# Optimization experiments

Hardware: AMD Instinct MI355X
Metric: run time of the kernel (lower is better)

The kernel has to match this reference:

```python
import jax, jax.numpy as jnp
import numpy as np

B = 16        # number of point clouds
NP = 4096     # points per cloud
RATIO = 0.25
RADIUS = 0.2
K = 64        # max_num_neighbors hardcoded in the torch module
S = int(NP * RATIO)  # sampled centers per cloud
C_IN = 64


def setup_inputs() -> dict:
    key = jax.random.key(0)
    ks = jax.random.split(key, 6)
    x = jax.random.normal(ks[0], (B * NP, C_IN), dtype=jnp.float32)
    pos = jax.random.uniform(ks[1], (B * NP, 3), dtype=jnp.float32)  # unit cube
    batch = jnp.repeat(jnp.arange(B, dtype=jnp.int64), NP)
    d0, d1, d2, d3 = C_IN + 3, 64, 64, 128  # local_nn dims
    W1 = jax.random.normal(ks[2], (d0, d1), dtype=jnp.float32) / np.sqrt(d0)
    W2 = jax.random.normal(ks[3], (d1, d2), dtype=jnp.float32) / np.sqrt(d1)
    W3 = jax.random.normal(ks[4], (d2, d3), dtype=jnp.float32) / np.sqrt(d2)
    b1 = jnp.zeros((d1,), jnp.float32)
    b2 = jnp.zeros((d2,), jnp.float32)
    b3 = jnp.zeros((d3,), jnp.float32)
    return {"x": x, "pos": pos, "batch": batch,
            "W1": W1, "b1": b1, "W2": W2, "b2": b2, "W3": W3, "b3": b3}


def _fps(pos_b):
    """Farthest point sampling for one cloud. pos_b: [NP,3] -> [S] int32 indices."""
    dmin = jnp.sum((pos_b - pos_b[0]) ** 2, axis=-1)  # start from point 0

    def step(dmin, _):
        idx = jnp.argmax(dmin).astype(jnp.int32)
        dmin = jnp.minimum(dmin, jnp.sum((pos_b - pos_b[idx]) ** 2, axis=-1))
        return dmin, idx

    _, idxs = jax.lax.scan(step, dmin, None, length=S - 1)
    return jnp.concatenate([jnp.zeros((1,), jnp.int32), idxs])


def reference(x, pos, batch, W1, b1, W2, b2, W3, b3):
    xb = x.reshape(B, NP, -1)
    pb = pos.reshape(B, NP, 3)

    def per_cloud(xb_, pb_):
        idxs = _fps(pb_)                      # [S]
        centers = pb_[idxs]                   # [S,3]
        # ball query: up to K nearest neighbors within RADIUS (center itself always in-range)
        d2 = jnp.sum((centers[:, None, :] - pb_[None, :, :]) ** 2, axis=-1)  # [S,NP]
        neg = jnp.where(d2 <= RADIUS * RADIUS, -d2, -jnp.inf)
        vals, nbr = jax.lax.top_k(neg, K)     # [S,K]
        valid = jnp.isfinite(vals)            # [S,K]
        # PointConv message: local_nn(concat(x_j, pos_j - pos_i)), max-aggregated
        xj = xb_[nbr]                         # [S,K,C]
        rel = pb_[nbr] - centers[:, None, :]  # [S,K,3]
        h = jnp.concatenate([xj, rel], axis=-1)
        h = jax.nn.relu(h @ W1 + b1)
        h = jax.nn.relu(h @ W2 + b2)
        h = h @ W3 + b3                       # [S,K,Cout]
        h = jnp.where(valid[..., None], h, -jnp.inf)
        return jnp.max(h, axis=1), centers    # [S,Cout], [S,3]

    out, centers = jax.vmap(per_cloud)(xb, pb)
    x_out = out.reshape(B * S, -1)
    pos_out = centers.reshape(B * S, 3)
    batch_out = jnp.repeat(jnp.arange(B, dtype=batch.dtype), S)
    return x_out, pos_out, batch_out
```

## Files before the change

### kernel.cpp

```cpp
#include <hip/hip_runtime.h>
#include <math.h>

#define NB   16
#define NPTS 4096
#define SS   1024
#define KK   64
#define CIN  64
#define TPB  512
#define NWORK 240
#define GRID (NB + NWORK)
#define WPREP_N 20480
#define BQCAP 768

typedef unsigned short ushort_t;
typedef float vf2 __attribute__((ext_vector_type(2)));
typedef unsigned long long vu2 __attribute__((ext_vector_type(2)));
typedef short bf8v __attribute__((ext_vector_type(8)));
typedef float f4v __attribute__((ext_vector_type(4)));

__device__ __forceinline__ float dist2(float ax, float ay, float az,
                                       float bx, float by, float bz) {
#pragma clang fp contract(off)
  float dx = ax - bx, dy = ay - by, dz = az - bz;
  float a = dx * dx, b = dy * dy, c = dz * dz;
  return (a + b) + c;
}

__device__ __forceinline__ vf2 dist2v(vf2 x, vf2 y, vf2 z,
                                      vf2 cx, vf2 cy, vf2 cz) {
#pragma clang fp contract(off)
  vf2 dx = x - cx, dy = y - cy, dz = z - cz;
  vf2 a = dx * dx, b = dy * dy, c = dz * dz;
  return (a + b) + c;
}

__device__ __forceinline__ ushort_t f2bf(float f) {
  unsigned u = __float_as_uint(f);
  return (ushort_t)((u + 0x7FFFu + ((u >> 16) & 1u)) >> 16);
}

#define DPPMAX(v, ctrl, rmask)                                                 \
  fmaxf((v), __int_as_float(__builtin_amdgcn_update_dpp(                       \
                 __float_as_int(v), __float_as_int(v), (ctrl), (rmask), 0xf,   \
                 false)))

__global__ __launch_bounds__(256) void wprep_kernel(
    const float* __restrict__ W1, const float* __restrict__ W2,
    const float* __restrict__ W3, ushort_t* __restrict__ wbuf) {
  int i = blockIdx.x * 256 + threadIdx.x;
  if (i >= WPREP_N) return;
  float v;
  if (i < 6656) {
    int n = i / 104, k = i - n * 104;
    v = (k < 67) ? W1[k * 64 + n] : 0.f;
  } else if (i < 11264) {
    int j = i - 6656;
    int n = j / 72, k = j - n * 72;
    v = (k < 64) ? W2[k * 64 + n] : 0.f;
  } else {
    int j = i - 11264;
    int n = j / 72, k = j - n * 72;
    v = (k < 64) ? W3[k * 128 + n] : 0.f;
  }
  wbuf[i] = f2bf(v);
}

struct FpsS {
  float px[NPTS], py[NPTS], pz[NPTS];
  unsigned long long swk[2][4];
};
struct WrkS {
  ushort_t feat[128][104];
  ushort_t h1[128][72];
  union {
    unsigned long long ckey[2 * BQCAP];
    ushort_t h2[128][72];
  } u;
  float red[8][128];
  int nbr_s[128];
  float cctr[6];
  int scnt[2];
};

__global__ __launch_bounds__(TPB) void fused_kernel(
    const float* __restrict__ pos, const float* __restrict__ x,
    const ushort_t* __restrict__ wbuf,
    const float* __restrict__ b1, const float* __restrict__ b2,
    const float* __restrict__ b3,
    float* __restrict__ centers4, int* __restrict__ prog,
    float* __restrict__ out_x, float* __restrict__ out_pos,
    float* __restrict__ out_batch) {
  __shared__ __align__(16) union { FpsS f; WrkS w; } S;
  const int t = threadIdx.x;

  if (blockIdx.x < NB) {
    asm volatile("s_setprio 3");
    const int b = blockIdx.x;
    const float* p = pos + (size_t)b * NPTS * 3;

    for (int j = t; j < NPTS * 3; j += TPB) {
      float v = p[j];
      int pt = j / 3, ch = j - pt * 3;
      if (ch == 0) S.f.px[pt] = v;
      else if (ch == 1) S.f.py[pt] = v;
      else S.f.pz[pt] = v;
    }
    for (int j = t; j < SS; j += TPB) out_batch[b * SS + j] = (float)b;
    __syncthreads();

    if (t < 256) {
      const int base = t * 16;
      vf2 x2[8], y2[8], z2[8], dm2[8];
      const float c0x = S.f.px[0], c0y = S.f.py[0], c0z = S.f.pz[0];
      {
        vf2 cX = {c0x, c0x}, cY = {c0y, c0y}, cZ = {c0z, c0z};
#pragma unroll
        for (int u = 0; u < 8; ++u) {
          x2[u].x = S.f.px[base + 2 * u]; x2[u].y = S.f.px[base + 2 * u + 1];
          y2[u].x = S.f.py[base + 2 * u]; y2[u].y = S.f.py[base + 2 * u + 1];
          z2[u].x = S.f.pz[base + 2 * u]; z2[u].y = S.f.pz[base + 2 * u + 1];
          dm2[u] = dist2v(x2[u], y2[u], z2[u], cX, cY, cZ);
        }
      }
      const int lane = t & 63, wid = t >> 6;
      const float BIG = 1e9f;
      int parity = 0;
      for (int s = 1; s < SS; ++s) {
        vf2 m0 = __builtin_elementwise_max(dm2[0], dm2[1]);
        vf2 m1 = __builtin_elementwise_max(dm2[2], dm2[3]);
        vf2 m2 = __builtin_elementwise_max(dm2[4], dm2[5]);
        vf2 m3 = __builtin_elementwise_max(dm2[6], dm2[7]);
        vf2 mm = __builtin_elementwise_max(
            __builtin_elementwise_max(m0, m1), __builtin_elementwise_max(m2, m3));
        float bv = fmaxf(mm.x, mm.y);
        float wv = bv;
        wv = DPPMAX(wv, 0x111, 0xf);
        wv = DPPMAX(wv, 0x112, 0xf);
        wv = DPPMAX(wv, 0x114, 0xf);
        wv = DPPMAX(wv, 0x118, 0xf);
        wv = DPPMAX(wv, 0x142, 0xa);
        wv = DPPMAX(wv, 0x143, 0xc);
        const float gvw =
            __int_as_float(__builtin_amdgcn_readlane(__float_as_int(wv), 63));
        unsigned long long mk = __ballot(bv == gvw);
        int fl = __ffsll((long long)mk) - 1;
        vf2 fcnt = {0.f, 1.f};
        vf2 best = {BIG, BIG};
#pragma unroll
        for (int u = 0; u < 8; ++u) {
          vf2 sv;
          sv.x = (dm2[u].x == gvw) ? fcnt.x : BIG;
          sv.y = (dm2[u].y == gvw) ? fcnt.y : BIG;
          best = __builtin_elementwise_min(best, sv);
          fcnt += (vf2){2.f, 2.f};
        }
        const int li = (int)fminf(best.x, best.y);
        if (lane == fl) {
          int gi = base + li;
          S.f.swk[parity][wid] =
              ((unsigned long long)__float_as_uint(gvw) << 32) |
              (unsigned)(~(unsigned)gi);
        }
        __syncthreads();
        const vu2* sp = (const vu2*)(&S.f.swk[parity][0]);
        vu2 q0 = sp[0], q1 = sp[1];
        unsigned long long bk = q0.x;
        bk = (q0.y > bk) ? q0.y : bk;
        bk = (q1.x > bk) ? q1.x : bk;
        bk = (q1.y > bk) ? q1.y : bk;
        const int gi = (int)(~(unsigned)bk);
        const float cx = S.f.px[gi], cy = S.f.py[gi], cz = S.f.pz[gi];
        {
          vf2 cX = {cx, cx}, cY = {cy, cy}, cZ = {cz, cz};
#pragma unroll
          for (int u = 0; u < 8; ++u) {
            vf2 d2 = dist2v(x2[u], y2[u], z2[u], cX, cY, cZ);
            dm2[u] = __builtin_elementwise_min(dm2[u], d2);
          }
        }
        parity ^= 1;
      }
      return;
    } else if (t < 320) {
      if (t == 256) {
        int r = b * SS;
        float c0x = S.f.px[0], c0y = S.f.py[0], c0z = S.f.pz[0];
        __hip_atomic_store(&centers4[r * 4 + 0], c0x, __ATOMIC_RELAXED, __HIP_MEMORY_SCOPE_AGENT);
        __hip_atomic_store(&centers4[r * 4 + 1], c0y, __ATOMIC_RELAXED, __HIP_MEMORY_SCOPE_AGENT);
        __hip_atomic_store(&centers4[r * 4 + 2], c0z, __ATOMIC_RELAXED, __HIP_MEMORY_SCOPE_AGENT);
        out_pos[r * 3 + 0] = c0x; out_pos[r * 3 + 1] = c0y; out_pos[r * 3 + 2] = c0z;
      }
      int parity = 0;
      for (int s = 1; s < SS; ++s) {
        __syncthreads();
        if (t == 256) {
          if ((s & 1) == 0) {
            asm volatile("s_waitcnt vmcnt(6)" ::: "memory");
            __hip_atomic_store(&prog[b * 32], s - 1, __ATOMIC_RELAXED, __HIP_MEMORY_SCOPE_AGENT);
          }
          const vu2* sp = (const vu2*)(&S.f.swk[parity][0]);
          vu2 q0 = sp[0], q1 = sp[1];
          unsigned long long bk = q0.x;
          bk = (q0.y > bk) ? q0.y : bk;
          bk = (q1.x > bk) ? q1.x : bk;
          bk = (q1.y > bk) ? q1.y : bk;
          const int gi = (int)(~(unsigned)bk);
          const float cx = S.f.px[gi], cy = S.f.py[gi], cz = S.f.pz[gi];
          int r = b * SS + s;
          __hip_atomic_store(&centers4[r * 4 + 0], cx, __ATOMIC_RELAXED, __HIP_MEMORY_SCOPE_AGENT);
          __hip_atomic_store(&centers4[r * 4 + 1], cy, __ATOMIC_RELAXED, __HIP_MEMORY_SCOPE_AGENT);
          __hip_atomic_store(&centers4[r * 4 + 2], cz, __ATOMIC_RELAXED, __HIP_MEMORY_SCOPE_AGENT);
          out_pos[r * 3 + 0] = cx; out_pos[r * 3 + 1] = cy; out_pos[r * 3 + 2] = cz;
        }
        parity ^= 1;
      }
      if (t == 256) {
        asm volatile("s_waitcnt vmcnt(0)" ::: "memory");
        __hip_atomic_store(&prog[b * 32], SS, __ATOMIC_RELAXED, __HIP_MEMORY_SCOPE_AGENT);
      }
      return;
    } else {
      for (int s = 1; s < SS; ++s) __syncthreads();
      return;
    }
  }

  const int w = blockIdx.x - NB;
  const int wv = t >> 6, lane = t & 63, lr = lane & 15, quad = lane >> 4;
  const int mrow = (wv << 4) + lr;
  const int mout = (wv << 4) + (quad << 2);
  const float R2 = 0.04f;

  for (int i = t; i < 128 * 14; i += TPB) {
    int r = i / 14, cp = i - r * 14;
    *(unsigned*)&S.w.feat[r][68 + 2 * cp] = 0;
  }
  if (t < 128) S.w.feat[t][67] = 0;

  for (int j = w; j < NB * SS / 2; j += NWORK) {
    const int sp = j >> 4, b = j & 15;
    const int s1 = sp * 2 + 1;
    const int c0 = b * SS + sp * 2, c1 = c0 + 1;
    if (t == 0) {
      while (__hip_atomic_load(&prog[b * 32], __ATOMIC_RELAXED,
                               __HIP_MEMORY_SCOPE_AGENT) <= s1)
        __builtin_amdgcn_s_sleep(2);
      S.w.cctr[0] = __hip_atomic_load(&centers4[c0 * 4 + 0], __ATOMIC_RELAXED, __HIP_MEMORY_SCOPE_AGENT);
      S.w.cctr[1] = __hip_atomic_load(&centers4[c0 * 4 + 1], __ATOMIC_RELAXED, __HIP_MEMORY_SCOPE_AGENT);
      S.w.cctr[2] = __hip_atomic_load(&centers4[c0 * 4 + 2], __ATOMIC_RELAXED, __HIP_MEMORY_SCOPE_AGENT);
      S.w.cctr[3] = __hip_atomic_load(&centers4[c1 * 4 + 0], __ATOMIC_RELAXED, __HIP_MEMORY_SCOPE_AGENT);
      S.w.cctr[4] = __hip_atomic_load(&centers4[c1 * 4 + 1], __ATOMIC_RELAXED, __HIP_MEMORY_SCOPE_AGENT);
      S.w.cctr[5] = __hip_atomic_load(&centers4[c1 * 4 + 2], __ATOMIC_RELAXED, __HIP_MEMORY_SCOPE_AGENT);
      S.w.scnt[0] = 0; S.w.scnt[1] = 0;
    }
    __syncthreads();
    const float cax = S.w.cctr[0], cay = S.w.cctr[1], caz = S.w.cctr[2];
    const float cbx = S.w.cctr[3], cby = S.w.cctr[4], cbz = S.w.cctr[5];
    const float* p = pos + (size_t)b * NPTS * 3;

#pragma unroll
    for (int ii = 0; ii < NPTS / TPB; ++ii) {
      const int i = t + ii * TPB;
      float ax = p[i * 3 + 0], ay = p[i * 3 + 1], az = p[i * 3 + 2];
      float dA = dist2(cax, cay, caz, ax, ay, az);
      float dB = dist2(cbx, cby, cbz, ax, ay, az);
      bool hA = (dA <= R2), hB = (dB <= R2);
      unsigned long long mA = __ballot(hA);
      if (mA) {
        int leader = __ffsll((long long)mA) - 1;
        int base = 0;
        if (lane == leader) base = atomicAdd(&S.w.scnt[0], __popcll(mA));
        base = __shfl(base, leader, 64);
        if (hA) {
          int off = base + (int)__popcll(mA & ((1ULL << lane) - 1ULL));
          if (off < BQCAP)
            S.w.u.ckey[off] =
                ((unsigned long long)__float_as_uint(dA) << 32) | (unsigned)i;
        }
      }
      unsigned long long mB = __ballot(hB);
      if (mB) {
        int leader = __ffsll((long long)mB) - 1;
        int base = 0;
        if (lane == leader) base = atomicAdd(&S.w.scnt[1], __popcll(mB));
        base = __shfl(base, leader, 64);
        if (hB) {
          int off = base + (int)__popcll(mB & ((1ULL << lane) - 1ULL));
          if (off < BQCAP)
            S.w.u.ckey[BQCAP + off] =
                ((unsigned long long)__float_as_uint(dB) << 32) | (unsigned)i;
        }
      }
    }
    __syncthreads();
    const int nvA = min(S.w.scnt[0], BQCAP), nvB = min(S.w.scnt[1], BQCAP);
    const int nvpA = (nvA + 15) & ~15, nvpB = (nvB + 15) & ~15;
    for (int q = nvA + t; q < nvpA; q += TPB) S.w.u.ckey[q] = ~0ULL;
    for (int q = nvB + t; q < nvpB; q += TPB) S.w.u.ckey[BQCAP + q] = ~0ULL;
    if (t < 128) S.w.nbr_s[t] = -1;
    __syncthreads();

    if (t < 256) {
      for (int sI = t; sI < nvA; sI += 256) {
        const unsigned long long k = S.w.u.ckey[sI];
        int r = 0;
        for (int q = 0; q < nvpA; q += 16) {
          const vu2* cp = (const vu2*)&S.w.u.ckey[q];
          vu2 a0 = cp[0], a1 = cp[1], a2 = cp[2], a3 = cp[3];
          vu2 a4 = cp[4], a5 = cp[5], a6 = cp[6], a7 = cp[7];
          r += (a0.x < k) + (a0.y < k) + (a1.x < k) + (a1.y < k);
          r += (a2.x < k) + (a2.y < k) + (a3.x < k) + (a3.y < k);
          r += (a4.x < k) + (a4.y < k) + (a5.x < k) + (a5.y < k);
          r += (a6.x < k) + (a6.y < k) + (a7.x < k) + (a7.y < k);
        }
        if (r < KK) S.w.nbr_s[r] = (int)(k & 0xFFFFFFFFu);
      }
    } else {
      const int t2 = t - 256;
      for (int sI = t2; sI < nvB; sI += 256) {
        const unsigned long long k = S.w.u.ckey[BQCAP + sI];
        int r = 0;
        for (int q = 0; q < nvpB; q += 16) {
          const vu2* cp = (const vu2*)&S.w.u.ckey[BQCAP + q];
          vu2 a0 = cp[0], a1 = cp[1], a2 = cp[2], a3 = cp[3];
          vu2 a4 = cp[4], a5 = cp[5], a6 = cp[6], a7 = cp[7];
          r += (a0.x < k) + (a0.y < k) + (a1.x < k) + (a1.y < k);
          r += (a2.x < k) + (a2.y < k) + (a3.x < k) + (a3.y < k);
          r += (a4.x < k) + (a4.y < k) + (a5.x < k) + (a5.y < k);
          r += (a6.x < k) + (a6.y < k) + (a7.x < k) + (a7.y < k);
        }
        if (r < KK) S.w.nbr_s[64 + r] = (int)(k & 0xFFFFFFFFu);
      }
    }
    __syncthreads();

    {
      const int c2 = t & 31;
#pragma unroll
      for (int kq = 0; kq < 8; ++kq) {
        const int k = (t >> 5) + kq * 16;
        const int li = S.w.nbr_s[k];
        const int li2 = (li < 0) ? 0 : li;
        const float* xp = x + ((size_t)(b * NPTS + li2)) * CIN + 2 * c2;
        float vx = xp[0], vy = xp[1];
        if (li < 0) { vx = 0.f; vy = 0.f; }
        unsigned pk = ((unsigned)f2bf(vy) << 16) | (unsigned)f2bf(vx);
        *(unsigned*)&S.w.feat[k][2 * c2] = pk;
      }
    }
    if (t < 128) {
      const int li = S.w.nbr_s[t];
      const int li2 = (li < 0) ? 0 : li;
      const float* pp = p + (size_t)li2 * 3;
      const float ccx = (t < 64) ? cax : cbx;
      const float ccy = (t < 64) ? cay : cby;
      const float ccz = (t < 64) ? caz : cbz;
      float rx = pp[0] - ccx, ry = pp[1] - ccy, rz = pp[2] - ccz;
      if (li < 0) { rx = 0.f; ry = 0.f; rz = 0.f; }
      S.w.feat[t][64] = f2bf(rx); S.w.feat[t][65] = f2bf(ry);
      S.w.feat[t][66] = f2bf(rz);
    }
    __syncthreads();

    {
      f4v acc[4] = {{0,0,0,0},{0,0,0,0},{0,0,0,0},{0,0,0,0}};
#pragma unroll
      for (int kb = 0; kb < 3; ++kb) {
        const int ko = kb * 32 + quad * 8;
        bf8v a = *(const bf8v*)&S.w.feat[mrow][ko];
#pragma unroll
        for (int nb = 0; nb < 4; ++nb) {
          bf8v bb = *(const bf8v*)&wbuf[(nb * 16 + lr) * 104 + ko];
          acc[nb] = __builtin_amdgcn_mfma_f32_16x16x32_bf16(a, bb, acc[nb], 0, 0, 0);
        }
      }
#pragma unroll
      for (int nb = 0; nb < 4; ++nb) {
        const int n = nb * 16 + lr;
        const float bias = b1[n];
#pragma unroll
        for (int r = 0; r < 4; ++r)
          S.w.h1[mout + r][n] = f2bf(fmaxf(acc[nb][r] + bias, 0.f));
      }
    }
    __syncthreads();

    {
      f4v acc[4] = {{0,0,0,0},{0,0,0,0},{0,0,0,0},{0,0,0,0}};
#pragma unroll
      for (int kb = 0; kb < 2; ++kb) {
        const int ko = kb * 32 + quad * 8;
        bf8v a = *(const bf8v*)&S.w.h1[mrow][ko];
#pragma unroll
        for (int nb = 0; nb < 4; ++nb) {
          bf8v bb = *(const bf8v*)&wbuf[6656 + (nb * 16 + lr) * 72 + ko];
          acc[nb] = __builtin_amdgcn_mfma_f32_16x16x32_bf16(a, bb, acc[nb], 0, 0, 0);
        }
      }
#pragma unroll
      for (int nb = 0; nb < 4; ++nb) {
        const int n = nb * 16 + lr;
        const float bias = b2[n];
#pragma unroll
        for (int r = 0; r < 4; ++r)
          S.w.u.h2[mout + r][n] = f2bf(fmaxf(acc[nb][r] + bias, 0.f));
      }
    }
    __syncthreads();

    {
      f4v acc[8] = {{0,0,0,0},{0,0,0,0},{0,0,0,0},{0,0,0,0},
                    {0,0,0,0},{0,0,0,0},{0,0,0,0},{0,0,0,0}};
#pragma unroll
      for (int kb = 0; kb < 2; ++kb) {
        const int ko = kb * 32 + quad * 8;
        bf8v a = *(const bf8v*)&S.w.u.h2[mrow][ko];
#pragma unroll
        for (int nb = 0; nb < 8; ++nb) {
          bf8v bb = *(const bf8v*)&wbuf[11264 + (nb * 16 + lr) * 72 + ko];
          acc[nb] = __builtin_amdgcn_mfma_f32_16x16x32_bf16(a, bb, acc[nb], 0, 0, 0);
        }
      }
      float vmax[8];
#pragma unroll
      for (int nb = 0; nb < 8; ++nb) vmax[nb] = -INFINITY;
#pragma unroll
      for (int r = 0; r < 4; ++r) {
        if (S.w.nbr_s[mout + r] >= 0) {
#pragma unroll
          for (int nb = 0; nb < 8; ++nb) vmax[nb] = fmaxf(vmax[nb], acc[nb][r]);
        }
      }
#pragma unroll
      for (int nb = 0; nb < 8; ++nb) {
        float v = vmax[nb];
        v = fmaxf(v, __shfl_xor(v, 16));
        v = fmaxf(v, __shfl_xor(v, 32));
        if (quad == 0) S.w.red[wv][nb * 16 + lr] = v;
      }
    }
    __syncthreads();

    if (t < 128) {
      float m = fmaxf(fmaxf(S.w.red[0][t], S.w.red[1][t]),
                      fmaxf(S.w.red[2][t], S.w.red[3][t]));
      out_x[(size_t)c0 * 128 + t] = m + b3[t];
    } else if (t < 256) {
      const int tt = t - 128;
      float m = fmaxf(fmaxf(S.w.red[4][tt], S.w.red[5][tt]),
                      fmaxf(S.w.red[6][tt], S.w.red[7][tt]));
      out_x[(size_t)c1 * 128 + tt] = m + b3[tt];
    }
  }
}

extern "C" void kernel_launch(void* const* d_in, const int* in_sizes, int n_in,
                              void* d_out, int out_size, void* d_ws, size_t ws_size,
                              hipStream_t stream) {
  const float* x   = (const float*)d_in[0];
  const float* pos = (const float*)d_in[1];
  const float* W1 = (const float*)d_in[3];
  const float* b1 = (const float*)d_in[4];
  const float* W2 = (const float*)d_in[5];
  const float* b2 = (const float*)d_in[6];
  const float* W3 = (const float*)d_in[7];
  const float* b3 = (const float*)d_in[8];

  float* centers4 = (float*)d_ws;
  int* prog       = (int*)(centers4 + (size_t)NB * SS * 4);
  ushort_t* wbuf  = (ushort_t*)(prog + NB * 32);

  float* out_x     = (float*)d_out;
  float* out_pos   = out_x + (size_t)NB * SS * 128;
  float* out_batch = out_pos + (size_t)NB * SS * 3;

  wprep_kernel<<<(WPREP_N + 255) / 256, 256, 0, stream>>>(W1, W2, W3, wbuf);
  fused_kernel<<<GRID, TPB, 0, stream>>>(pos, x, wbuf, b1, b2, b3,
                                         centers4, prog,
                                         out_x, out_pos, out_batch);
}
```

Baseline: 752.5 us.

## Pack two FPS clouds per producer block and publish centers from a compute wave

Producer blocks now each run farthest-point sampling for two clouds, using four waves per cloud instead of one cloud per block with idle waves. This halves the number of producer blocks and frees CUs for the neighbor/MLP worker blocks. The separate publisher wave is removed: a lane of each cloud's first wave writes the centers and updates progress, now every fourth step with a full vmcnt(0) wait. The risk is that the two clouds share one __syncthreads per step and the compute wave absorbs the publishing stores, which may lengthen the serial FPS critical path and delay the consumers.

```diff
diff --git a/kernel.cpp b/kernel.cpp
--- a/kernel.cpp
+++ b/kernel.cpp
@@ -7,8 +7,9 @@
 #define KK   64
 #define CIN  64
 #define TPB  512
+#define NPROD 8
 #define NWORK 240
-#define GRID (NB + NWORK)
+#define GRID (NPROD + NWORK)
 #define WPREP_N 20480
 #define BQCAP 768
 
@@ -66,8 +67,8 @@
 }
 
 struct FpsS {
-  float px[NPTS], py[NPTS], pz[NPTS];
-  unsigned long long swk[2][4];
+  float px[2][NPTS], py[2][NPTS], pz[2][NPTS];
+  unsigned long long swk[2][2][4];
 };
 struct WrkS {
   ushort_t feat[128][104];
@@ -93,139 +94,127 @@
   __shared__ __align__(16) union { FpsS f; WrkS w; } S;
   const int t = threadIdx.x;
 
-  if (blockIdx.x < NB) {
+  if (blockIdx.x < NPROD) {
     asm volatile("s_setprio 3");
-    const int b = blockIdx.x;
-    const float* p = pos + (size_t)b * NPTS * 3;
-
-    for (int j = t; j < NPTS * 3; j += TPB) {
-      float v = p[j];
-      int pt = j / 3, ch = j - pt * 3;
-      if (ch == 0) S.f.px[pt] = v;
-      else if (ch == 1) S.f.py[pt] = v;
-      else S.f.pz[pt] = v;
-    }
-    for (int j = t; j < SS; j += TPB) out_batch[b * SS + j] = (float)b;
-    __syncthreads();
-
-    if (t < 256) {
-      const int base = t * 16;
-      vf2 x2[8], y2[8], z2[8], dm2[8];
-      const float c0x = S.f.px[0], c0y = S.f.py[0], c0z = S.f.pz[0];
+    const int cA = blockIdx.x * 2;
+
+    for (int j = t; j < NPTS * 3 * 2; j += TPB) {
+      const int cl = j / (NPTS * 3);
+      const int jj = j - cl * NPTS * 3;
+      float v = pos[(size_t)(cA + cl) * NPTS * 3 + jj];
+      int pt = jj / 3, ch = jj - pt * 3;
+      if (ch == 0) S.f.px[cl][pt] = v;
+      else if (ch == 1) S.f.py[cl][pt] = v;
+      else S.f.pz[cl][pt] = v;
+    }
+    for (int j = t; j < 2 * SS; j += TPB) {
+      const int cl = j >> 10;
+      out_batch[(size_t)(cA + cl) * SS + (j & 1023)] = (float)(cA + cl);
+    }
+    __syncthreads();
+
+    const int wv = t >> 6, lane = t & 63;
+    const int g = wv >> 2, wg = wv & 3;
+    const int b = cA + g;
+    const int base = (wg * 64 + lane) * 16;
+    const bool pub = (wg == 0 && lane == 0);
+
+    vf2 x2[8], y2[8], z2[8], dm2[8];
+    const float c0x = S.f.px[g][0], c0y = S.f.py[g][0], c0z = S.f.pz[g][0];
+    {
+      vf2 cX = {c0x, c0x}, cY = {c0y, c0y}, cZ = {c0z, c0z};
+#pragma unroll
+      for (int u = 0; u < 8; ++u) {
+        x2[u].x = S.f.px[g][base + 2 * u]; x2[u].y = S.f.px[g][base + 2 * u + 1];
+        y2[u].x = S.f.py[g][base + 2 * u]; y2[u].y = S.f.py[g][base + 2 * u + 1];
+        z2[u].x = S.f.pz[g][base + 2 * u]; z2[u].y = S.f.pz[g][base + 2 * u + 1];
+        dm2[u] = dist2v(x2[u], y2[u], z2[u], cX, cY, cZ);
+      }
+    }
+    if (pub) {
+      int r = b * SS;
+      __hip_atomic_store(&centers4[r * 4 + 0], c0x, __ATOMIC_RELAXED, __HIP_MEMORY_SCOPE_AGENT);
+      __hip_atomic_store(&centers4[r * 4 + 1], c0y, __ATOMIC_RELAXED, __HIP_MEMORY_SCOPE_AGENT);
+      __hip_atomic_store(&centers4[r * 4 + 2], c0z, __ATOMIC_RELAXED, __HIP_MEMORY_SCOPE_AGENT);
+      out_pos[r * 3 + 0] = c0x; out_pos[r * 3 + 1] = c0y; out_pos[r * 3 + 2] = c0z;
+    }
+
+    const float BIG = 1e9f;
+    int parity = 0;
+    for (int s = 1; s < SS; ++s) {
+      vf2 m0 = __builtin_elementwise_max(dm2[0], dm2[1]);
+      vf2 m1 = __builtin_elementwise_max(dm2[2], dm2[3]);
+      vf2 m2 = __builtin_elementwise_max(dm2[4], dm2[5]);
+      vf2 m3 = __builtin_elementwise_max(dm2[6], dm2[7]);
+      vf2 mm = __builtin_elementwise_max(
+          __builtin_elementwise_max(m0, m1), __builtin_elementwise_max(m2, m3));
+      float bv = fmaxf(mm.x, mm.y);
+      float wvx = bv;
+      wvx = DPPMAX(wvx, 0x111, 0xf);
+      wvx = DPPMAX(wvx, 0x112, 0xf);
+      wvx = DPPMAX(wvx, 0x114, 0xf);
+      wvx = DPPMAX(wvx, 0x118, 0xf);
+      wvx = DPPMAX(wvx, 0x142, 0xa);
+      wvx = DPPMAX(wvx, 0x143, 0xc);
+      const float gvw =
+          __int_as_float(__builtin_amdgcn_readlane(__float_as_int(wvx), 63));
+      unsigned long long mk = __ballot(bv == gvw);
+      int fl = __ffsll((long long)mk) - 1;
+      vf2 fcnt = {0.f, 1.f};
+      vf2 best = {BIG, BIG};
+#pragma unroll
+      for (int u = 0; u < 8; ++u) {
+        vf2 sv;
+        sv.x = (dm2[u].x == gvw) ? fcnt.x : BIG;
+        sv.y = (dm2[u].y == gvw) ? fcnt.y : BIG;
+        best = __builtin_elementwise_min(best, sv);
+        fcnt += (vf2){2.f, 2.f};
+      }
+      const int li = (int)fminf(best.x, best.y);
+      if (lane == fl) {
+        int gi = base + li;
+        S.f.swk[parity][g][wg] =
+            ((unsigned long long)__float_as_uint(gvw) << 32) |
+            (unsigned)(~(unsigned)gi);
+      }
+      __syncthreads();
+      const vu2* sp = (const vu2*)(&S.f.swk[parity][g][0]);
+      vu2 q0 = sp[0], q1 = sp[1];
+      unsigned long long bk = q0.x;
+      bk = (q0.y > bk) ? q0.y : bk;
+      bk = (q1.x > bk) ? q1.x : bk;
+      bk = (q1.y > bk) ? q1.y : bk;
+      const int gi = (int)(~(unsigned)bk);
+      const float cx = S.f.px[g][gi], cy = S.f.py[g][gi], cz = S.f.pz[g][gi];
+      if (pub) {
+        if ((s & 3) == 0) {
+          asm volatile("s_waitcnt vmcnt(0)" ::: "memory");
+          __hip_atomic_store(&prog[b * 32], s, __ATOMIC_RELAXED, __HIP_MEMORY_SCOPE_AGENT);
+        }
+        int r = b * SS + s;
+        __hip_atomic_store(&centers4[r * 4 + 0], cx, __ATOMIC_RELAXED, __HIP_MEMORY_SCOPE_AGENT);
+        __hip_atomic_store(&centers4[r * 4 + 1], cy, __ATOMIC_RELAXED, __HIP_MEMORY_SCOPE_AGENT);
+        __hip_atomic_store(&centers4[r * 4 + 2], cz, __ATOMIC_RELAXED, __HIP_MEMORY_SCOPE_AGENT);
+        out_pos[r * 3 + 0] = cx; out_pos[r * 3 + 1] = cy; out_pos[r * 3 + 2] = cz;
+      }
       {
-        vf2 cX = {c0x, c0x}, cY = {c0y, c0y}, cZ = {c0z, c0z};
+        vf2 cX = {cx, cx}, cY = {cy, cy}, cZ = {cz, cz};
 #pragma unroll
         for (int u = 0; u < 8; ++u) {
-          x2[u].x = S.f.px[base + 2 * u]; x2[u].y = S.f.px[base + 2 * u + 1];
-          y2[u].x = S.f.py[base + 2 * u]; y2[u].y = S.f.py[base + 2 * u + 1];
-          z2[u].x = S.f.pz[base + 2 * u]; z2[u].y = S.f.pz[base + 2 * u + 1];
-          dm2[u] = dist2v(x2[u], y2[u], z2[u], cX, cY, cZ);
-        }
-      }
-      const int lane = t & 63, wid = t >> 6;
-      const float BIG = 1e9f;
-      int parity = 0;
-      for (int s = 1; s < SS; ++s) {
-        vf2 m0 = __builtin_elementwise_max(dm2[0], dm2[1]);
-        vf2 m1 = __builtin_elementwise_max(dm2[2], dm2[3]);
-        vf2 m2 = __builtin_elementwise_max(dm2[4], dm2[5]);
-        vf2 m3 = __builtin_elementwise_max(dm2[6], dm2[7]);
-        vf2 mm = __builtin_elementwise_max(
-            __builtin_elementwise_max(m0, m1), __builtin_elementwise_max(m2, m3));
-        float bv = fmaxf(mm.x, mm.y);
-        float wv = bv;
-        wv = DPPMAX(wv, 0x111, 0xf);
-        wv = DPPMAX(wv, 0x112, 0xf);
-        wv = DPPMAX(wv, 0x114, 0xf);
-        wv = DPPMAX(wv, 0x118, 0xf);
-        wv = DPPMAX(wv, 0x142, 0xa);
-        wv = DPPMAX(wv, 0x143, 0xc);
-        const float gvw =
-            __int_as_float(__builtin_amdgcn_readlane(__float_as_int(wv), 63));
-        unsigned long long mk = __ballot(bv == gvw);
-        int fl = __ffsll((long long)mk) - 1;
-        vf2 fcnt = {0.f, 1.f};
-        vf2 best = {BIG, BIG};
-#pragma unroll
-        for (int u = 0; u < 8; ++u) {
-          vf2 sv;
-          sv.x = (dm2[u].x == gvw) ? fcnt.x : BIG;
-          sv.y = (dm2[u].y == gvw) ? fcnt.y : BIG;
-          best = __builtin_elementwise_min(best, sv);
-          fcnt += (vf2){2.f, 2.f};
-        }
-        const int li = (int)fminf(best.x, best.y);
-        if (lane == fl) {
-          int gi = base + li;
-          S.f.swk[parity][wid] =
-              ((unsigned long long)__float_as_uint(gvw) << 32) |
-              (unsigned)(~(unsigned)gi);
-        }
-        __syncthreads();
-        const vu2* sp = (const vu2*)(&S.f.swk[parity][0]);
-        vu2 q0 = sp[0], q1 = sp[1];
-        unsigned long long bk = q0.x;
-        bk = (q0.y > bk) ? q0.y : bk;
-        bk = (q1.x > bk) ? q1.x : bk;
-        bk = (q1.y > bk) ? q1.y : bk;
-        const int gi = (int)(~(unsigned)bk);
-        const float cx = S.f.px[gi], cy = S.f.py[gi], cz = S.f.pz[gi];
-        {
-          vf2 cX = {cx, cx}, cY = {cy, cy}, cZ = {cz, cz};
-#pragma unroll
-          for (int u = 0; u < 8; ++u) {
-            vf2 d2 = dist2v(x2[u], y2[u], z2[u], cX, cY, cZ);
-            dm2[u] = __builtin_elementwise_min(dm2[u], d2);
-          }
-        }
-        parity ^= 1;
-      }
-      return;
-    } else if (t < 320) {
-      if (t == 256) {
-        int r = b * SS;
-        float c0x = S.f.px[0], c0y = S.f.py[0], c0z = S.f.pz[0];
-        __hip_atomic_store(&centers4[r * 4 + 0], c0x, __ATOMIC_RELAXED, __HIP_MEMORY_SCOPE_AGENT);
-        __hip_atomic_store(&centers4[r * 4 + 1], c0y, __ATOMIC_RELAXED, __HIP_MEMORY_SCOPE_AGENT);
-        __hip_atomic_store(&centers4[r * 4 + 2], c0z, __ATOMIC_RELAXED, __HIP_MEMORY_SCOPE_AGENT);
-        out_pos[r * 3 + 0] = c0x; out_pos[r * 3 + 1] = c0y; out_pos[r * 3 + 2] = c0z;
-      }
-      int parity = 0;
-      for (int s = 1; s < SS; ++s) {
-        __syncthreads();
-        if (t == 256) {
-          if ((s & 1) == 0) {
-            asm volatile("s_waitcnt vmcnt(6)" ::: "memory");
-            __hip_atomic_store(&prog[b * 32], s - 1, __ATOMIC_RELAXED, __HIP_MEMORY_SCOPE_AGENT);
-          }
-          const vu2* sp = (const vu2*)(&S.f.swk[parity][0]);
-          vu2 q0 = sp[0], q1 = sp[1];
-          unsigned long long bk = q0.x;
-          bk = (q0.y > bk) ? q0.y : bk;
-          bk = (q1.x > bk) ? q1.x : bk;
-          bk = (q1.y > bk) ? q1.y : bk;
-          const int gi = (int)(~(unsigned)bk);
-          const float cx = S.f.px[gi], cy = S.f.py[gi], cz = S.f.pz[gi];
-          int r = b * SS + s;
-          __hip_atomic_store(&centers4[r * 4 + 0], cx, __ATOMIC_RELAXED, __HIP_MEMORY_SCOPE_AGENT);
-          __hip_atomic_store(&centers4[r * 4 + 1], cy, __ATOMIC_RELAXED, __HIP_MEMORY_SCOPE_AGENT);
-          __hip_atomic_store(&centers4[r * 4 + 2], cz, __ATOMIC_RELAXED, __HIP_MEMORY_SCOPE_AGENT);
-          out_pos[r * 3 + 0] = cx; out_pos[r * 3 + 1] = cy; out_pos[r * 3 + 2] = cz;
-        }
-        parity ^= 1;
-      }
-      if (t == 256) {
-        asm volatile("s_waitcnt vmcnt(0)" ::: "memory");
-        __hip_atomic_store(&prog[b * 32], SS, __ATOMIC_RELAXED, __HIP_MEMORY_SCOPE_AGENT);
-      }
-      return;
-    } else {
-      for (int s = 1; s < SS; ++s) __syncthreads();
-      return;
-    }
+          vf2 d2 = dist2v(x2[u], y2[u], z2[u], cX, cY, cZ);
+          dm2[u] = __builtin_elementwise_min(dm2[u], d2);
+        }
+      }
+      parity ^= 1;
+    }
+    if (pub) {
+      asm volatile("s_waitcnt vmcnt(0)" ::: "memory");
+      __hip_atomic_store(&prog[b * 32], SS, __ATOMIC_RELAXED, __HIP_MEMORY_SCOPE_AGENT);
+    }
+    return;
   }
 
-  const int w = blockIdx.x - NB;
+  const int w = blockIdx.x - NPROD;
   const int wv = t >> 6, lane = t & 63, lr = lane & 15, quad = lane >> 4;
   const int mrow = (wv << 4) + lr;
   const int mout = (wv << 4) + (quad << 2);
```

New measurement: 1.032 ms. 1.37x slower.
